# Performance work log

Measured on AMD Instinct MI355X. Metric: run time of the kernel, lower is better.

## Reference

```python
import jax, jax.numpy as jnp
import numpy as np

N = 729        # problem variables
B = 8          # batch
K = 32         # mixing rank (hard-coded in MixingFunc)
NB = 40        # number of symmetry-basis matrices
MAX_ITER = 10  # coordinate-descent sweeps


def setup_inputs() -> dict:
    key = jax.random.key(0)
    ks = jax.random.split(key, 7)
    coeff = jax.random.normal(ks[0], (NB,), jnp.float32)
    upper = jax.random.normal(ks[1], (N,), jnp.float32)
    basis = jax.random.normal(ks[2], (NB, N, N), jnp.float32)
    z = jax.random.uniform(ks[3], (B, N), jnp.float32)
    is_input = jax.random.randint(ks[4], (B, N), 0, 2).astype(jnp.int32)
    v_init_raw = jax.random.normal(ks[5], (B, N + 1, K), jnp.float32)
    # random permutation of the N non-truth variables (indices 1..N), as in satnet init
    perm = (jax.random.permutation(ks[6], N) + 1).astype(jnp.int32)
    return dict(coeff=coeff, upper=upper, basis=basis, z=z,
                is_input=is_input, v_init_raw=v_init_raw, perm=perm)


def _build_C(coeff, upper, basis):
    # BasisFunc.forward: C = [[0, upper^T], [upper, sum_b coeff_b * basis_b]]
    center = jnp.einsum('b,bij->ij', coeff, basis)              # (N, N)
    top = jnp.concatenate([jnp.zeros((1,), upper.dtype), upper])[None, :]  # (1, N+1)
    bottom = jnp.concatenate([upper[:, None], center], axis=1)  # (N, N+1)
    return jnp.concatenate([top, bottom], axis=0)               # (N+1, N+1)


def _init_V(v_raw, z_full):
    # SATNet init: v0 = random unit truth direction; each v_i is placed on the
    # cone around v0 at angle pi*z_i using a random orthogonal direction.
    v0 = v_raw[:, 0] / jnp.linalg.norm(v_raw[:, 0], axis=-1, keepdims=True)  # (B, K)
    dot = jnp.einsum('bnk,bk->bn', v_raw, v0)
    u = v_raw - dot[..., None] * v0[:, None, :]
    u = u / jnp.maximum(jnp.linalg.norm(u, axis=-1, keepdims=True), 1e-8)
    c = jnp.cos(jnp.pi * z_full)[..., None]
    s = jnp.sin(jnp.pi * z_full)[..., None]
    V = -c * v0[:, None, :] + s * u                              # (B, N+1, K)
    V = V.at[:, 0].set(v0)                                       # truth vector pinned
    return V


def _mix(C, V, is_input_full, perm):
    # SATNet mixing coordinate descent: for each free variable i,
    #   g_i = sum_j C[j,i] v_j - C[i,i] v_i ;  v_i <- -g_i / ||g_i||
    Cdiag = jnp.diagonal(C)
    free = (is_input_full == 0)                                  # (B, N+1)

    def coord_step(V, i):
        g = jnp.einsum('j,bjk->bk', C[:, i], V) - Cdiag[i] * V[:, i]  # (B, K)
        gn = jnp.linalg.norm(g, axis=-1, keepdims=True)
        vnew = -g / jnp.maximum(gn, 1e-8)
        V = V.at[:, i].set(jnp.where(free[:, i][:, None], vnew, V[:, i]))
        return V, None

    def sweep(V, _):
        V, _ = jax.lax.scan(coord_step, V, perm)
        return V, None

    V, _ = jax.lax.scan(jax.checkpoint(sweep), V, None, length=MAX_ITER)
    return V


def reference(coeff, upper, basis, z, is_input, v_init_raw, perm):
    Bn = z.shape[0]
    C = _build_C(coeff, upper, basis)
    z_full = jnp.concatenate([jnp.ones((Bn, 1), z.dtype), z], axis=1)
    ii_full = jnp.concatenate(
        [jnp.ones((Bn, 1), is_input.dtype), is_input], axis=1)
    V = _init_V(v_init_raw, z_full)
    V = _mix(C, V, ii_full, perm)
    v0 = V[:, 0]
    cosang = jnp.clip(-jnp.einsum('bnk,bk->bn', V, v0), -1.0 + 1e-6, 1.0 - 1e-6)
    zo = jnp.arccos(cosang) / jnp.pi
    z_out = jnp.where(ii_full == 1, z_full, zo)
    return z_out[:, 1:]
```

## Files before the change

kernel.cpp:

```cpp
#include <hip/hip_runtime.h>

#define NN   729
#define NF   730
#define BV   8
#define KK   32
#define NBAS 40
#define MAXIT 10
#define PI_F 3.14159265358979323846f

#define MTH   512
#define BT    16
#define AST   448

typedef float v2f __attribute__((ext_vector_type(2)));

__device__ __forceinline__ void fma4(float4& w, float c, const float4& d) {
    w.x = fmaf(c, d.x, w.x); w.y = fmaf(c, d.y, w.y);
    w.z = fmaf(c, d.z, w.z); w.w = fmaf(c, d.w, w.w);
}

__global__ void build_C_kernel(const float* __restrict__ coeff,
                               const float* __restrict__ upper,
                               const float* __restrict__ basis,
                               float* __restrict__ Ct) {
    int idx = blockIdx.x * blockDim.x + threadIdx.x;
    if (idx >= NF * NF) return;
    int i = idx / NF, j = idx - i * NF;
    float val;
    if (i == 0) {
        val = (j == 0) ? 0.f : upper[j - 1];
    } else if (j == 0) {
        val = upper[i - 1];
    } else {
        float acc = 0.f;
        const float* bp = basis + (size_t)(i - 1) * NN + (j - 1);
        #pragma unroll 8
        for (int b = 0; b < NBAS; ++b)
            acc = fmaf(coeff[b], bp[(size_t)b * NN * NN], acc);
        val = acc;
    }
    Ct[(size_t)j * NF + i] = val;
}

__global__ void init_V_kernel(const float* __restrict__ z,
                              const float* __restrict__ vraw,
                              float* __restrict__ V) {
    int g = threadIdx.x >> 5;
    int k = threadIdx.x & 31;
    int row = blockIdx.x * 8 + g;
    int b = row / NF, n = row - b * NF;
    const float* vr = vraw + (size_t)b * NF * KK;

    float v0 = vr[k];
    float s2 = v0 * v0;
    #pragma unroll
    for (int off = 16; off; off >>= 1) s2 += __shfl_xor(s2, off, 32);
    v0 = v0 / sqrtf(s2);

    float vn = vr[(size_t)n * KK + k];
    float d = vn * v0;
    #pragma unroll
    for (int off = 16; off; off >>= 1) d += __shfl_xor(d, off, 32);
    float u = vn - d * v0;
    float un2 = u * u;
    #pragma unroll
    for (int off = 16; off; off >>= 1) un2 += __shfl_xor(un2, off, 32);
    u = u / fmaxf(sqrtf(un2), 1e-8f);

    float zf = (n == 0) ? 1.f : z[b * NN + (n - 1)];
    float c = cosf(PI_F * zf), s = sinf(PI_F * zf);
    float outv = -c * v0 + s * u;
    if (n == 0) outv = v0;
    V[((size_t)b * NF + n) * KK + k] = outv;
}

__global__ void build_act_kernel(const int* __restrict__ is_input,
                                 const int* __restrict__ perm,
                                 int* __restrict__ act, int* __restrict__ nA_arr) {
    int b = blockIdx.x, l = threadIdx.x;
    int base = 0;
    for (int c = 0; c < (NN + 63) / 64; ++c) {
        int idx = c * 64 + l;
        bool f = false; int pi = 0;
        if (idx < NN) { pi = perm[idx]; f = (is_input[b * NN + pi - 1] == 0); }
        unsigned long long m = __ballot(f);
        int pos = __popcll(m & ((1ull << l) - 1ull));
        if (f && base + pos < AST) act[b * AST + base + pos] = pi;
        base += __popcll(m);
    }
    if (base > AST) base = AST;
    if (l == 0) nA_arr[b] = base;
    for (int p = base + l; p < AST; p += 64) act[b * AST + p] = 0;
}

__global__ void gather_CactT_kernel(const float* __restrict__ Ct,
                                    const int* __restrict__ act,
                                    float* __restrict__ CactT) {
    int a = blockIdx.x, b = blockIdx.y;
    __shared__ int acts[AST];
    for (int i = threadIdx.x; i < AST; i += blockDim.x) acts[i] = act[b * AST + i];
    __syncthreads();
    const float* src = Ct + (size_t)acts[a] * NF;
    float* dst = CactT + ((size_t)b * AST + a) * AST;
    for (int t = threadIdx.x; t < AST; t += blockDim.x)
        dst[t] = src[acts[t]];
}

__global__ void init_W_kernel(const float* __restrict__ Ct,
                              const int* __restrict__ act,
                              const int* __restrict__ nA_arr,
                              const float* __restrict__ V,
                              float* __restrict__ Wc,
                              float* __restrict__ Vact) {
    int b = blockIdx.y;
    int a = blockIdx.x * 8 + (threadIdx.x >> 5);
    int k = threadIdx.x & 31;
    int nA = nA_arr[b];
    float w = 0.f;
    int ra = act[b * AST + a];
    float vv = V[((size_t)b * NF + ra) * KK + k];
    if (a < nA) {
        const float* ctr = Ct + (size_t)ra * NF;
        const float* vb = V + (size_t)b * NF * KK + k;
        float acc = 0.f;
        for (int j = 0; j < NF; ++j)
            acc = fmaf(ctr[j], vb[(size_t)j * KK], acc);
        w = acc - ctr[ra] * vv;
    }
    Wc[((size_t)b * AST + a) * KK + k] = w;
    Vact[((size_t)b * AST + a) * KK + k] = vv;
}

__device__ __forceinline__ float rowsum16(float x) {
    int y;
    y = __builtin_amdgcn_update_dpp(0, __float_as_int(x), 0x121, 0xF, 0xF, false);
    x += __int_as_float(y);
    y = __builtin_amdgcn_update_dpp(0, __float_as_int(x), 0x122, 0xF, 0xF, false);
    x += __int_as_float(y);
    y = __builtin_amdgcn_update_dpp(0, __float_as_int(x), 0x124, 0xF, 0xF, false);
    x += __int_as_float(y);
    y = __builtin_amdgcn_update_dpp(0, __float_as_int(x), 0x128, 0xF, 0xF, false);
    x += __int_as_float(y);
    return x;
}

__global__ __launch_bounds__(MTH, 2)
void mix_kernel(const float* __restrict__ CactT_g,
                const float* __restrict__ Wc_g,
                const float* __restrict__ Vact_g,
                const int* __restrict__ act_g,
                const int* __restrict__ nA_arr,
                const int* __restrict__ is_input,
                const float* __restrict__ z,
                const float* __restrict__ Vg,
                float* __restrict__ out) {
    __shared__ __align__(16) float V_c[AST * KK];
    __shared__ __align__(16) float dv_s[2][BT * KK];
    __shared__ __align__(16) float gpub[2][BT * KK];
    __shared__ __align__(16) float cblk_s[2][BT * BT];
    __shared__ __align__(16) float cmini_s[BT * BT];
    __shared__ float Cd_s[AST];
    __shared__ int   slot_s[NF];

    int b = blockIdx.x, tid = threadIdx.x;
    const float* CT = CactT_g + (size_t)b * AST * AST;
    const float* Vact = Vact_g + (size_t)b * AST * KK;
    int nA = nA_arr[b];
    int nblkp = (nA + BT - 1) / BT;
    if (nblkp < 2) nblkp = 2;
    int nAp = nblkp * BT;
    int totB = MAXIT * nblkp;

    int wid = tid >> 6;
    int l64 = tid & 63;
    int lane = tid - 64;
    int kq = lane & 7;
    int rslot = lane >> 3;
    int kp = tid & 15;

    for (int idx = tid; idx < AST * 8; idx += MTH)
        ((float4*)V_c)[idx] = ((const float4*)Vact)[idx];
    if (tid < AST) Cd_s[tid] = CT[(size_t)tid * AST + tid];
    if (tid < nA) slot_s[act_g[b * AST + tid]] = tid;
    if (tid < 256) {
        int t = tid >> 4, u = tid & 15;
        cblk_s[0][t * BT + u] = CT[(size_t)u * AST + t];
    }
    float4 w[8];
    #pragma unroll
    for (int p = 0; p < 8; ++p) {
        float4 zz = {0.f, 0.f, 0.f, 0.f};
        w[p] = zz;
        if (wid >= 1)
            w[p] = *(const float4*)&Wc_g[((size_t)b * AST + rslot + 56 * p) * KK + 4 * kq];
    }
    if (wid >= 1) {
        #pragma unroll
        for (int p = 0; p < 8; ++p) {
            int a = rslot + 56 * p;
            if ((a >> 4) == 0)
                *(float4*)&gpub[1][a * KK + 4 * kq] = w[p];
        }
    }
    __syncthreads();

    for (int bi = 0; bi < totB; ++bi) {
        int blk = bi % nblkp, s0 = blk * BT;
        int pblk = (bi - 1 + nblkp) % nblkp, sp0 = pblk * BT;
        int cb = bi & 1, pv = cb ^ 1;
        int nblk2 = (bi + 1) % nblkp, sn0 = nblk2 * BT;

        if (wid == 0) {
            float g0[BT], g1[BT], vo0[BT], vo1[BT];
            #pragma unroll
            for (int u = 0; u < BT; ++u) {
                v2f gv = *(const v2f*)&gpub[pv][u * KK + 2 * kp];
                g0[u] = gv.x; g1[u] = gv.y;
                v2f vv = *(const v2f*)&V_c[(s0 + u) * KK + 2 * kp];
                vo0[u] = vv.x; vo1[u] = vv.y;
            }
            #pragma unroll
            for (int u = 0; u < BT; ++u) {
                int s = s0 + u;
                float n2 = fmaf(g0[u], g0[u], g1[u] * g1[u]);
                n2 = rowsum16(n2);
                float inv = -__builtin_amdgcn_rsqf(fmaxf(n2, 1e-16f));
                float msk = (s < nA) ? 1.f : 0.f;
                float d0 = fmaf(g0[u], inv, -vo0[u]) * msk;
                float d1 = fmaf(g1[u], inv, -vo1[u]) * msk;
                if (tid < 16) {
                    v2f dv2; dv2.x = d0; dv2.y = d1;
                    *(v2f*)&dv_s[cb][u * KK + 2 * kp] = dv2;
                    v2f vn2; vn2.x = vo0[u] + d0; vn2.y = vo1[u] + d1;
                    *(v2f*)&V_c[s * KK + 2 * kp] = vn2;
                }
                #pragma unroll
                for (int u2 = u + 1; u2 < BT; ++u2) {
                    float c = cblk_s[cb][u * BT + u2];
                    g0[u2] = fmaf(c, d0, g0[u2]);
                    g1[u2] = fmaf(c, d1, g1[u2]);
                }
            }
        } else {
            if (wid == 6) {
                int u = l64 & 15, q = l64 >> 4;
                float4 v = *(const float4*)&CT[(size_t)(sn0 + u) * AST + s0 + 4 * q];
                *(float4*)&cmini_s[u * BT + 4 * q] = v;
            }
            if (wid == 7) {
                int u = l64 & 15, q = l64 >> 4;
                float4 v = *(const float4*)&CT[(size_t)(sn0 + u) * AST + sn0 + 4 * q];
                cblk_s[pv][(4 * q + 0) * BT + u] = v.x;
                cblk_s[pv][(4 * q + 1) * BT + u] = v.y;
                cblk_s[pv][(4 * q + 2) * BT + u] = v.z;
                cblk_s[pv][(4 * q + 3) * BT + u] = v.w;
            }
            if (bi > 0) {
                #pragma unroll
                for (int h = 0; h < 2; ++h) {
                    float4 dvv[8];
                    #pragma unroll
                    for (int t = 0; t < 8; ++t)
                        dvv[t] = *(const float4*)&dv_s[pv][(8 * h + t) * KK + 4 * kq];
                    float4 cA0, cB0, cA1, cB1;
                    {
                        const float* cr = CT + (size_t)rslot * AST + sp0 + 8 * h;
                        cA0 = *(const float4*)(cr);
                        cB0 = *(const float4*)(cr + 4);
                    }
                    #pragma unroll
                    for (int p = 0; p < 8; ++p) {
                        int a = rslot + 56 * p;
                        if (p < 7) {
                            const float* cr = CT + (size_t)(a + 56) * AST + sp0 + 8 * h;
                            if (p & 1) { cA0 = *(const float4*)(cr); cB0 = *(const float4*)(cr + 4); }
                            else       { cA1 = *(const float4*)(cr); cB1 = *(const float4*)(cr + 4); }
                        }
                        float4 ca = (p & 1) ? cA1 : cA0;
                        float4 cbq = (p & 1) ? cB1 : cB0;
                        if (a < nAp) {
                            fma4(w[p], ca.x,  dvv[0]);
                            fma4(w[p], ca.y,  dvv[1]);
                            fma4(w[p], ca.z,  dvv[2]);
                            fma4(w[p], ca.w,  dvv[3]);
                            fma4(w[p], cbq.x, dvv[4]);
                            fma4(w[p], cbq.y, dvv[5]);
                            fma4(w[p], cbq.z, dvv[6]);
                            fma4(w[p], cbq.w, dvv[7]);
                        }
                    }
                }
                #pragma unroll
                for (int p = 0; p < 8; ++p) {
                    int a = rslot + 56 * p;
                    if ((a >> 4) == pblk) {
                        float4 dd = *(const float4*)&dv_s[pv][(a - sp0) * KK + 4 * kq];
                        fma4(w[p], -Cd_s[a], dd);
                    }
                }
            }
            #pragma unroll
            for (int p = 0; p < 8; ++p) {
                int a = rslot + 56 * p;
                if ((a >> 4) == nblk2)
                    *(float4*)&gpub[cb][(a - sn0) * KK + 4 * kq] = w[p];
            }
        }
        __syncthreads();

        {
            int u = tid >> 5, k = tid & 31;
            float g = gpub[cb][u * KK + k];
            #pragma unroll
            for (int t = 0; t < BT; ++t)
                g = fmaf(cmini_s[u * BT + t], dv_s[cb][t * KK + k], g);
            gpub[cb][u * KK + k] = g;
        }
        __syncthreads();
    }

    int k = tid & 31, r = tid >> 5;
    float v0k = Vg[(size_t)b * NF * KK + k];
    for (int n = 1 + r; n <= NN; n += 16) {
        int ii = is_input[b * NN + n - 1];
        float res;
        if (ii == 1) {
            res = z[b * NN + n - 1];
        } else {
            int a = slot_s[n];
            float dot = V_c[a * KK + k] * v0k;
            #pragma unroll
            for (int off = 16; off; off >>= 1) dot += __shfl_xor(dot, off, 32);
            float ca = fminf(fmaxf(-dot, -1.f + 1e-6f), 1.f - 1e-6f);
            res = acosf(ca) * (1.f / PI_F);
        }
        if (k == 0) out[b * NN + n - 1] = res;
    }
}

extern "C" void kernel_launch(void* const* d_in, const int* in_sizes, int n_in,
                              void* d_out, int out_size, void* d_ws, size_t ws_size,
                              hipStream_t stream) {
    const float* coeff    = (const float*)d_in[0];
    const float* upper    = (const float*)d_in[1];
    const float* basis    = (const float*)d_in[2];
    const float* z        = (const float*)d_in[3];
    const int*   is_input = (const int*)d_in[4];
    const float* vraw     = (const float*)d_in[5];
    const int*   perm     = (const int*)d_in[6];
    float* out = (float*)d_out;

    float* ws    = (float*)d_ws;
    float* Ct    = ws;
    float* V     = Ct + (size_t)NF * NF;
    float* CactT = V + (size_t)BV * NF * KK;
    float* Wc    = CactT + (size_t)BV * AST * AST;
    float* Vact  = Wc + (size_t)BV * AST * KK;
    int*   act   = (int*)(Vact + (size_t)BV * AST * KK);
    int*   nAa   = act + BV * AST;

    build_C_kernel<<<dim3((NF * NF + 255) / 256), dim3(256), 0, stream>>>(coeff, upper, basis, Ct);
    init_V_kernel<<<dim3(730), dim3(256), 0, stream>>>(z, vraw, V);
    build_act_kernel<<<dim3(BV), dim3(64), 0, stream>>>(is_input, perm, act, nAa);
    gather_CactT_kernel<<<dim3(AST, BV), dim3(256), 0, stream>>>(Ct, act, CactT);
    init_W_kernel<<<dim3(AST / 8, BV), dim3(256), 0, stream>>>(Ct, act, nAa, V, Wc, Vact);
    mix_kernel<<<dim3(BV), dim3(MTH), 0, stream>>>(CactT, Wc, Vact, act, nAa, is_input, z, V, out);
}
```

Measured before the change: 743.6 us.

## Double the coordinate-descent block size to 32 and use full-wave lanes per row

Raises the blocked coordinate-descent tile from 16 to 32 variables, halving the number of block iterations and __syncthreads pairs per sweep. The serial wave-0 solver now uses 32 lanes with one K element each instead of 16 lanes with two, adding a shuffle to the norm reduction. The staging, mini-correction and rank-update loops are widened to match. In exchange the serial triangular update inside each block gets longer and uses more registers, and the padding of the active set to a multiple of 32 adds wasted work.

Result: slower. 2.701 ms (+263.2%).

```diff
diff --git a/kernel.cpp b/kernel.cpp
--- a/kernel.cpp
+++ b/kernel.cpp
@@ -9,7 +9,7 @@
 #define PI_F 3.14159265358979323846f
 
 #define MTH   512
-#define BT    16
+#define BT    32
 #define AST   448
 
 typedef float v2f __attribute__((ext_vector_type(2)));
@@ -176,15 +176,15 @@
     int lane = tid - 64;
     int kq = lane & 7;
     int rslot = lane >> 3;
-    int kp = tid & 15;
+    int k32 = tid & 31;
 
     for (int idx = tid; idx < AST * 8; idx += MTH)
         ((float4*)V_c)[idx] = ((const float4*)Vact)[idx];
     if (tid < AST) Cd_s[tid] = CT[(size_t)tid * AST + tid];
     if (tid < nA) slot_s[act_g[b * AST + tid]] = tid;
-    if (tid < 256) {
-        int t = tid >> 4, u = tid & 15;
-        cblk_s[0][t * BT + u] = CT[(size_t)u * AST + t];
+    for (int idx = tid; idx < BT * BT; idx += MTH) {
+        int x = idx >> 5, y = idx & 31;
+        cblk_s[0][idx] = CT[(size_t)y * AST + x];
     }
     float4 w[8];
     #pragma unroll
@@ -198,7 +198,7 @@
         #pragma unroll
         for (int p = 0; p < 8; ++p) {
             int a = rslot + 56 * p;
-            if ((a >> 4) == 0)
+            if ((a >> 5) == 0)
                 *(float4*)&gpub[1][a * KK + 4 * kq] = w[p];
         }
     }
@@ -211,60 +211,62 @@
         int nblk2 = (bi + 1) % nblkp, sn0 = nblk2 * BT;
 
         if (wid == 0) {
-            float g0[BT], g1[BT], vo0[BT], vo1[BT];
+            float g[BT], vo[BT];
             #pragma unroll
             for (int u = 0; u < BT; ++u) {
-                v2f gv = *(const v2f*)&gpub[pv][u * KK + 2 * kp];
-                g0[u] = gv.x; g1[u] = gv.y;
-                v2f vv = *(const v2f*)&V_c[(s0 + u) * KK + 2 * kp];
-                vo0[u] = vv.x; vo1[u] = vv.y;
+                g[u]  = gpub[pv][u * KK + k32];
+                vo[u] = V_c[(s0 + u) * KK + k32];
             }
             #pragma unroll
             for (int u = 0; u < BT; ++u) {
                 int s = s0 + u;
-                float n2 = fmaf(g0[u], g0[u], g1[u] * g1[u]);
+                float n2 = g[u] * g[u];
                 n2 = rowsum16(n2);
+                n2 += __shfl_xor(n2, 16, 32);
                 float inv = -__builtin_amdgcn_rsqf(fmaxf(n2, 1e-16f));
                 float msk = (s < nA) ? 1.f : 0.f;
-                float d0 = fmaf(g0[u], inv, -vo0[u]) * msk;
-                float d1 = fmaf(g1[u], inv, -vo1[u]) * msk;
-                if (tid < 16) {
-                    v2f dv2; dv2.x = d0; dv2.y = d1;
-                    *(v2f*)&dv_s[cb][u * KK + 2 * kp] = dv2;
-                    v2f vn2; vn2.x = vo0[u] + d0; vn2.y = vo1[u] + d1;
-                    *(v2f*)&V_c[s * KK + 2 * kp] = vn2;
-                }
-                #pragma unroll
-                for (int u2 = u + 1; u2 < BT; ++u2) {
-                    float c = cblk_s[cb][u * BT + u2];
-                    g0[u2] = fmaf(c, d0, g0[u2]);
-                    g1[u2] = fmaf(c, d1, g1[u2]);
-                }
+                float d = fmaf(g[u], inv, -vo[u]) * msk;
+                if (tid < 32) {
+                    dv_s[cb][u * KK + k32] = d;
+                    V_c[s * KK + k32] = vo[u] + d;
+                }
+                #pragma unroll
+                for (int u2 = u + 1; u2 < BT; ++u2)
+                    g[u2] = fmaf(cblk_s[cb][u * BT + u2], d, g[u2]);
             }
         } else {
             if (wid == 6) {
-                int u = l64 & 15, q = l64 >> 4;
-                float4 v = *(const float4*)&CT[(size_t)(sn0 + u) * AST + s0 + 4 * q];
-                *(float4*)&cmini_s[u * BT + 4 * q] = v;
+                #pragma unroll
+                for (int q = 0; q < 4; ++q) {
+                    int idx = q * 64 + l64;
+                    int u = idx >> 3, tq = idx & 7;
+                    float4 v = *(const float4*)&CT[(size_t)(sn0 + u) * AST + s0 + 4 * tq];
+                    *(float4*)&cmini_s[u * BT + 4 * tq] = v;
+                }
             }
             if (wid == 7) {
-                int u = l64 & 15, q = l64 >> 4;
-                float4 v = *(const float4*)&CT[(size_t)(sn0 + u) * AST + sn0 + 4 * q];
-                cblk_s[pv][(4 * q + 0) * BT + u] = v.x;
-                cblk_s[pv][(4 * q + 1) * BT + u] = v.y;
-                cblk_s[pv][(4 * q + 2) * BT + u] = v.z;
-                cblk_s[pv][(4 * q + 3) * BT + u] = v.w;
+                #pragma unroll
+                for (int q = 0; q < 4; ++q) {
+                    int idx = q * 64 + l64;
+                    int u = idx >> 3, xq = idx & 7;
+                    float4 v = *(const float4*)&CT[(size_t)(sn0 + u) * AST + sn0 + 4 * xq];
+                    cblk_s[pv][(4 * xq + 0) * BT + u] = v.x;
+                    cblk_s[pv][(4 * xq + 1) * BT + u] = v.y;
+                    cblk_s[pv][(4 * xq + 2) * BT + u] = v.z;
+                    cblk_s[pv][(4 * xq + 3) * BT + u] = v.w;
+                }
             }
             if (bi > 0) {
                 #pragma unroll
-                for (int h = 0; h < 2; ++h) {
+                for (int qt = 0; qt < 4; ++qt) {
                     float4 dvv[8];
                     #pragma unroll
                     for (int t = 0; t < 8; ++t)
-                        dvv[t] = *(const float4*)&dv_s[pv][(8 * h + t) * KK + 4 * kq];
+                        dvv[t] = *(const float4*)&dv_s[pv][(8 * qt + t) * KK + 4 * kq];
+                    const float* cq = CT + sp0 + 8 * qt;
                     float4 cA0, cB0, cA1, cB1;
                     {
-                        const float* cr = CT + (size_t)rslot * AST + sp0 + 8 * h;
+                        const float* cr = cq + (size_t)rslot * AST;
                         cA0 = *(const float4*)(cr);
                         cB0 = *(const float4*)(cr + 4);
                     }
@@ -272,7 +274,7 @@
                     for (int p = 0; p < 8; ++p) {
                         int a = rslot + 56 * p;
                         if (p < 7) {
-                            const float* cr = CT + (size_t)(a + 56) * AST + sp0 + 8 * h;
+                            const float* cr = cq + (size_t)(a + 56) * AST;
                             if (p & 1) { cA0 = *(const float4*)(cr); cB0 = *(const float4*)(cr + 4); }
                             else       { cA1 = *(const float4*)(cr); cB1 = *(const float4*)(cr + 4); }
                         }
@@ -293,7 +295,7 @@
                 #pragma unroll
                 for (int p = 0; p < 8; ++p) {
                     int a = rslot + 56 * p;
-                    if ((a >> 4) == pblk) {
+                    if ((a >> 5) == pblk) {
                         float4 dd = *(const float4*)&dv_s[pv][(a - sp0) * KK + 4 * kq];
                         fma4(w[p], -Cd_s[a], dd);
                     }
@@ -302,19 +304,24 @@
             #pragma unroll
             for (int p = 0; p < 8; ++p) {
                 int a = rslot + 56 * p;
-                if ((a >> 4) == nblk2)
+                if ((a >> 5) == nblk2)
                     *(float4*)&gpub[cb][(a - sn0) * KK + 4 * kq] = w[p];
             }
         }
         __syncthreads();
 
         {
-            int u = tid >> 5, k = tid & 31;
-            float g = gpub[cb][u * KK + k];
-            #pragma unroll
-            for (int t = 0; t < BT; ++t)
-                g = fmaf(cmini_s[u * BT + t], dv_s[cb][t * KK + k], g);
-            gpub[cb][u * KK + k] = g;
+            int k = tid & 31;
+            int u0 = tid >> 5;
+            #pragma unroll
+            for (int uu = 0; uu < 2; ++uu) {
+                int u = u0 + 16 * uu;
+                float g = gpub[cb][u * KK + k];
+                #pragma unroll
+                for (int t = 0; t < BT; ++t)
+                    g = fmaf(cmini_s[u * BT + t], dv_s[cb][t * KK + k], g);
+                gpub[cb][u * KK + k] = g;
+            }
         }
         __syncthreads();
     }
```
